# Optimization experiments

Measured on AMD Instinct MI355X. Metric: run time of the kernel, lower is better.

The kernel has to match this reference:

```python
import jax, jax.numpy as jnp
import numpy as np

EPS = 1e-12  # F.normalize eps


def setup_inputs() -> dict:
    key = jax.random.key(0)
    B, T, D = 1024, 32, 1024
    inputs = jax.random.normal(key, (B, T, D), dtype=jnp.float32)
    return {"inputs": inputs}


def reference(inputs) -> jnp.ndarray:
    # L2-normalize each frame embedding along D (torch F.normalize, p=2, dim=2)
    norm = jnp.maximum(jnp.linalg.norm(inputs, axis=2, keepdims=True), EPS)
    inputs_normed = inputs / norm                     # [B, T, D]
    mean_rep = jnp.mean(inputs_normed, axis=1)        # [B, D]
    # Original loops over T computing matmul(...).diag(); equivalent to a
    # per-sample dot product of each frame with its own clip mean.
    dots = jnp.einsum("btd,bd->bt", inputs_normed, mean_rep)  # [B, T]
    dist = jnp.sum(1.0 - dots, axis=1)                # [B]
    return jnp.mean(dist)
```

## Files before the change

### kernel.cpp

```cpp
#include <hip/hip_runtime.h>


#define TT 32
#define DD 1024
#define BB 1024

__global__ __launch_bounds__(512, 4) void clip_partial_kernel(
    const float* __restrict__ x, float* __restrict__ partial) {
  const int b = blockIdx.x;
  const float* __restrict__ xb = x + (size_t)b * (TT * DD);
  const int lane = threadIdx.x & 63;
  const int wave = threadIdx.x >> 6;

  __shared__ float4 sacc[8 * 4 * 64];
  __shared__ float wsum[4];

  float4 v[4][4];
#pragma unroll
  for (int r = 0; r < 4; ++r)
#pragma unroll
    for (int i = 0; i < 4; ++i)
      v[r][i] = *reinterpret_cast<const float4*>(xb + (wave * 4 + r) * DD +
                                                 i * 256 + lane * 4);

#pragma unroll
  for (int r = 0; r < 4; ++r)
#pragma unroll
    for (int i = 0; i < 4; ++i)
      asm volatile("" : "+v"(v[r][i].x), "+v"(v[r][i].y), "+v"(v[r][i].z),
                       "+v"(v[r][i].w));

  float inv[4];
#pragma unroll
  for (int r = 0; r < 4; ++r) {
    float ss = 0.0f;
#pragma unroll
    for (int i = 0; i < 4; ++i)
      ss += v[r][i].x * v[r][i].x + v[r][i].y * v[r][i].y +
            v[r][i].z * v[r][i].z + v[r][i].w * v[r][i].w;
#pragma unroll
    for (int off = 32; off; off >>= 1) ss += __shfl_xor(ss, off);
    inv[r] = 1.0f / fmaxf(sqrtf(ss), 1e-12f);
  }

#pragma unroll
  for (int i = 0; i < 4; ++i) {
    float4 a = make_float4(0.f, 0.f, 0.f, 0.f);
#pragma unroll
    for (int r = 0; r < 4; ++r) {
      a.x = fmaf(v[r][i].x, inv[r], a.x);
      a.y = fmaf(v[r][i].y, inv[r], a.y);
      a.z = fmaf(v[r][i].z, inv[r], a.z);
      a.w = fmaf(v[r][i].w, inv[r], a.w);
    }
    sacc[(wave * 4 + i) * 64 + lane] = a;
  }
  __syncthreads();

  float local = 0.0f;
  if (threadIdx.x < 256) {
    const int i = threadIdx.x >> 6;
    float4 s4 = make_float4(0.f, 0.f, 0.f, 0.f);
#pragma unroll
    for (int w = 0; w < 8; ++w) {
      const float4 t4 = sacc[(w * 4 + i) * 64 + lane];
      s4.x += t4.x;
      s4.y += t4.y;
      s4.z += t4.z;
      s4.w += t4.w;
    }
    local = s4.x * s4.x + s4.y * s4.y + s4.z * s4.z + s4.w * s4.w;
  }
#pragma unroll
  for (int off = 32; off; off >>= 1) local += __shfl_xor(local, off);
  if (wave < 4 && lane == 0) wsum[wave] = local;
  __syncthreads();
  if (threadIdx.x == 0) {
    const float s2 = wsum[0] + wsum[1] + wsum[2] + wsum[3];
    partial[b] = (float)TT - s2 * (1.0f / (float)TT);
  }
}

__global__ __launch_bounds__(256) void clip_reduce_kernel(
    const float* __restrict__ partial, float* __restrict__ out) {
  const int lane = threadIdx.x & 63;
  const int wave = threadIdx.x >> 6;
  const float4 v =
      *reinterpret_cast<const float4*>(partial + threadIdx.x * 4);
  float s = v.x + v.y + v.z + v.w;
#pragma unroll
  for (int off = 32; off; off >>= 1) s += __shfl_xor(s, off);
  __shared__ float wsum[4];
  if (lane == 0) wsum[wave] = s;
  __syncthreads();
  if (threadIdx.x == 0)
    out[0] = (wsum[0] + wsum[1] + wsum[2] + wsum[3]) * (1.0f / (float)BB);
}

extern "C" void kernel_launch(void* const* d_in, const int* in_sizes, int n_in,
                              void* d_out, int out_size, void* d_ws,
                              size_t ws_size, hipStream_t stream) {
  const float* x = (const float*)d_in[0];
  float* partial = (float*)d_ws;
  float* out = (float*)d_out;

  clip_partial_kernel<<<BB, 512, 0, stream>>>(x, partial);
  clip_reduce_kernel<<<1, 256, 0, stream>>>(partial, out);
}
```

Before: 27.75 us.

## Process two samples per block and prefetch the second during the first's reduction

The grid is halved so each block handles samples b and b+512. The second sample's global loads are issued into registers before the first sample's shared-memory reduction and barriers, so that memory latency overlaps the reduction. In exchange, half as many blocks are resident, which lowers memory-level parallelism from occupancy, and the kernel does more serial work per block.

```diff
diff --git a/kernel.cpp b/kernel.cpp
--- a/kernel.cpp
+++ b/kernel.cpp
@@ -4,31 +4,35 @@
 #define TT 32
 #define DD 1024
 #define BB 1024
+#define GRID 512
+
+#define PIN4(f4) \
+  asm volatile("" : "+v"((f4).x), "+v"((f4).y), "+v"((f4).z), "+v"((f4).w))
 
 __global__ __launch_bounds__(512, 4) void clip_partial_kernel(
     const float* __restrict__ x, float* __restrict__ partial) {
-  const int b = blockIdx.x;
-  const float* __restrict__ xb = x + (size_t)b * (TT * DD);
   const int lane = threadIdx.x & 63;
   const int wave = threadIdx.x >> 6;
 
   __shared__ float4 sacc[8 * 4 * 64];
   __shared__ float wsum[4];
 
+  const int b0 = blockIdx.x;
+  const int b1 = blockIdx.x + GRID;
+  const float* __restrict__ xb0 = x + (size_t)b0 * (TT * DD);
+  const float* __restrict__ xb1 = x + (size_t)b1 * (TT * DD);
+
   float4 v[4][4];
 #pragma unroll
   for (int r = 0; r < 4; ++r)
 #pragma unroll
     for (int i = 0; i < 4; ++i)
-      v[r][i] = *reinterpret_cast<const float4*>(xb + (wave * 4 + r) * DD +
+      v[r][i] = *reinterpret_cast<const float4*>(xb0 + (wave * 4 + r) * DD +
                                                  i * 256 + lane * 4);
-
 #pragma unroll
   for (int r = 0; r < 4; ++r)
 #pragma unroll
-    for (int i = 0; i < 4; ++i)
-      asm volatile("" : "+v"(v[r][i].x), "+v"(v[r][i].y), "+v"(v[r][i].z),
-                       "+v"(v[r][i].w));
+    for (int i = 0; i < 4; ++i) PIN4(v[r][i]);
 
   float inv[4];
 #pragma unroll
@@ -42,42 +46,105 @@
     for (int off = 32; off; off >>= 1) ss += __shfl_xor(ss, off);
     inv[r] = 1.0f / fmaxf(sqrtf(ss), 1e-12f);
   }
+  float4 a[4];
+#pragma unroll
+  for (int i = 0; i < 4; ++i) {
+    a[i] = make_float4(0.f, 0.f, 0.f, 0.f);
+#pragma unroll
+    for (int r = 0; r < 4; ++r) {
+      a[i].x = fmaf(v[r][i].x, inv[r], a[i].x);
+      a[i].y = fmaf(v[r][i].y, inv[r], a[i].y);
+      a[i].z = fmaf(v[r][i].z, inv[r], a[i].z);
+      a[i].w = fmaf(v[r][i].w, inv[r], a[i].w);
+    }
+  }
 
 #pragma unroll
+  for (int r = 0; r < 4; ++r)
+#pragma unroll
+    for (int i = 0; i < 4; ++i)
+      v[r][i] = *reinterpret_cast<const float4*>(xb1 + (wave * 4 + r) * DD +
+                                                 i * 256 + lane * 4);
+
+#pragma unroll
+  for (int i = 0; i < 4; ++i) sacc[(wave * 4 + i) * 64 + lane] = a[i];
+  __syncthreads();
+  {
+    float local = 0.0f;
+    if (threadIdx.x < 256) {
+      const int i = threadIdx.x >> 6;
+      float4 s4 = make_float4(0.f, 0.f, 0.f, 0.f);
+#pragma unroll
+      for (int w = 0; w < 8; ++w) {
+        const float4 t4 = sacc[(w * 4 + i) * 64 + lane];
+        s4.x += t4.x;
+        s4.y += t4.y;
+        s4.z += t4.z;
+        s4.w += t4.w;
+      }
+      local = s4.x * s4.x + s4.y * s4.y + s4.z * s4.z + s4.w * s4.w;
+    }
+#pragma unroll
+    for (int off = 32; off; off >>= 1) local += __shfl_xor(local, off);
+    if (wave < 4 && lane == 0) wsum[wave] = local;
+    __syncthreads();
+    if (threadIdx.x == 0)
+      partial[b0] =
+          (float)TT - (wsum[0] + wsum[1] + wsum[2] + wsum[3]) / (float)TT;
+  }
+
+#pragma unroll
+  for (int r = 0; r < 4; ++r)
+#pragma unroll
+    for (int i = 0; i < 4; ++i) PIN4(v[r][i]);
+
+#pragma unroll
+  for (int r = 0; r < 4; ++r) {
+    float ss = 0.0f;
+#pragma unroll
+    for (int i = 0; i < 4; ++i)
+      ss += v[r][i].x * v[r][i].x + v[r][i].y * v[r][i].y +
+            v[r][i].z * v[r][i].z + v[r][i].w * v[r][i].w;
+#pragma unroll
+    for (int off = 32; off; off >>= 1) ss += __shfl_xor(ss, off);
+    inv[r] = 1.0f / fmaxf(sqrtf(ss), 1e-12f);
+  }
+#pragma unroll
   for (int i = 0; i < 4; ++i) {
-    float4 a = make_float4(0.f, 0.f, 0.f, 0.f);
+    a[i] = make_float4(0.f, 0.f, 0.f, 0.f);
 #pragma unroll
     for (int r = 0; r < 4; ++r) {
-      a.x = fmaf(v[r][i].x, inv[r], a.x);
-      a.y = fmaf(v[r][i].y, inv[r], a.y);
-      a.z = fmaf(v[r][i].z, inv[r], a.z);
-      a.w = fmaf(v[r][i].w, inv[r], a.w);
+      a[i].x = fmaf(v[r][i].x, inv[r], a[i].x);
+      a[i].y = fmaf(v[r][i].y, inv[r], a[i].y);
+      a[i].z = fmaf(v[r][i].z, inv[r], a[i].z);
+      a[i].w = fmaf(v[r][i].w, inv[r], a[i].w);
     }
-    sacc[(wave * 4 + i) * 64 + lane] = a;
-  }
-  __syncthreads();
-
-  float local = 0.0f;
-  if (threadIdx.x < 256) {
-    const int i = threadIdx.x >> 6;
-    float4 s4 = make_float4(0.f, 0.f, 0.f, 0.f);
-#pragma unroll
-    for (int w = 0; w < 8; ++w) {
-      const float4 t4 = sacc[(w * 4 + i) * 64 + lane];
-      s4.x += t4.x;
-      s4.y += t4.y;
-      s4.z += t4.z;
-      s4.w += t4.w;
-    }
-    local = s4.x * s4.x + s4.y * s4.y + s4.z * s4.z + s4.w * s4.w;
   }
 #pragma unroll
-  for (int off = 32; off; off >>= 1) local += __shfl_xor(local, off);
-  if (wave < 4 && lane == 0) wsum[wave] = local;
+  for (int i = 0; i < 4; ++i) sacc[(wave * 4 + i) * 64 + lane] = a[i];
   __syncthreads();
-  if (threadIdx.x == 0) {
-    const float s2 = wsum[0] + wsum[1] + wsum[2] + wsum[3];
-    partial[b] = (float)TT - s2 * (1.0f / (float)TT);
+  {
+    float local = 0.0f;
+    if (threadIdx.x < 256) {
+      const int i = threadIdx.x >> 6;
+      float4 s4 = make_float4(0.f, 0.f, 0.f, 0.f);
+#pragma unroll
+      for (int w = 0; w < 8; ++w) {
+        const float4 t4 = sacc[(w * 4 + i) * 64 + lane];
+        s4.x += t4.x;
+        s4.y += t4.y;
+        s4.z += t4.z;
+        s4.w += t4.w;
+      }
+      local = s4.x * s4.x + s4.y * s4.y + s4.z * s4.z + s4.w * s4.w;
+    }
+#pragma unroll
+    for (int off = 32; off; off >>= 1) local += __shfl_xor(local, off);
+    if (wave < 4 && lane == 0) wsum[wave] = local;
+    __syncthreads();
+    if (threadIdx.x == 0)
+      partial[b1] =
+          (float)TT - (wsum[0] + wsum[1] + wsum[2] + wsum[3]) / (float)TT;
   }
 }
 
@@ -104,6 +171,6 @@
   float* partial = (float*)d_ws;
   float* out = (float*)d_out;
 
-  clip_partial_kernel<<<BB, 512, 0, stream>>>(x, partial);
+  clip_partial_kernel<<<GRID, 512, 0, stream>>>(x, partial);
   clip_reduce_kernel<<<1, 256, 0, stream>>>(partial, out);
 }
```

Result: slower. 28.42 us (+2.4%).
